# Performance work log

Hardware: AMD Instinct MI355X
Metric: run time of the kernel (lower is better)

The kernel has to match this reference:

```python
import jax, jax.numpy as jnp
import numpy as np

N = 50000   # nodes per graph
E = 800000  # edges per graph
D = 128     # in_dim (num_features)
H = 128     # hidden_channels
R = 8       # num_etypes


def setup_inputs() -> dict:
    key = jax.random.key(0)
    ks = jax.random.split(key, 32)
    inp = {}
    inp["x1"] = jax.random.normal(ks[0], (N, D), dtype=jnp.float32)
    inp["edge_index1"] = jax.random.randint(ks[1], (2, E), 0, N)
    inp["edge_type1"] = jnp.sort(jax.random.randint(ks[2], (E,), 0, R))
    inp["x2"] = jax.random.normal(ks[3], (N, D), dtype=jnp.float32)
    inp["edge_index2"] = jax.random.randint(ks[4], (2, E), 0, N)
    inp["edge_type2"] = jnp.sort(jax.random.randint(ks[5], (E,), 0, R))
    # RGCNConv params: relation weights [R, in, out], root weight [in, out], bias [out]
    dims = [(D, H), (H, H), (H, H)]
    k = 6
    for l, (di, do) in enumerate(dims):
        s = 1.0 / np.sqrt(di)
        inp[f"W{l}"] = jax.random.normal(ks[k], (R, di, do), dtype=jnp.float32) * s; k += 1
        inp[f"root{l}"] = jax.random.normal(ks[k], (di, do), dtype=jnp.float32) * s; k += 1
        inp[f"bias{l}"] = jnp.zeros((do,), dtype=jnp.float32)
    # FCL: MLP on concat(u1, u2) of width 2*H -> H -> 1 (assumed architecture)
    s = 1.0 / np.sqrt(2 * H)
    inp["fc1_w"] = jax.random.normal(ks[k], (2 * H, H), dtype=jnp.float32) * s; k += 1
    inp["fc1_b"] = jnp.zeros((H,), dtype=jnp.float32)
    s = 1.0 / np.sqrt(H)
    inp["fc2_w"] = jax.random.normal(ks[k], (H, 1), dtype=jnp.float32) * s; k += 1
    inp["fc2_b"] = jnp.zeros((1,), dtype=jnp.float32)
    return inp


def rgcn_conv(x, src, dst, etype, W, root, bias):
    # PyG RGCNConv: out_i = root @ x_i + bias + sum_r mean_{j in N_r(i)} W_r x_j
    # transform all nodes by all relation weights: [R, N, H]
    t = jnp.einsum('nd,rdh->rnh', x, W)
    msg = t[etype, src]                       # [E, H] per-edge gathered messages
    comb = dst * R + etype                    # combined (node, relation) segment id
    cnt = jax.ops.segment_sum(jnp.ones((E,), x.dtype), comb, num_segments=N * R)
    msg = msg * (1.0 / jnp.maximum(cnt, 1.0))[comb][:, None]  # per-relation mean norm
    agg = jax.ops.segment_sum(msg, dst, num_segments=N)       # scatter-add over relations
    return agg + x @ root + bias


def gnn(x, edge_index, edge_type, params):
    src, dst = edge_index[0], edge_index[1]
    u = jax.nn.relu(rgcn_conv(x, src, dst, edge_type, *params[0]))
    u = jax.nn.relu(rgcn_conv(u, src, dst, edge_type, *params[1]))
    u = rgcn_conv(u, src, dst, edge_type, *params[2])
    return jnp.mean(u, axis=0).reshape(1, -1)  # [1, H]


def reference(x1, edge_index1, edge_type1, x2, edge_index2, edge_type2,
              W0, root0, bias0, W1, root1, bias1, W2, root2, bias2,
              fc1_w, fc1_b, fc2_w, fc2_b):
    params = [(W0, root0, bias0), (W1, root1, bias1), (W2, root2, bias2)]
    u1 = gnn(x1, edge_index1, edge_type1, params)
    u2 = gnn(x2, edge_index2, edge_type2, params)
    h = jnp.concatenate([u1, u2], axis=-1)    # [1, 2H]
    return jax.nn.relu(h @ fc1_w + fc1_b) @ fc2_w + fc2_b  # [1, 1]
```

## Files before the change

### kernel.cpp

```cpp
#include <hip/hip_runtime.h>

#define R_ET 8
#define DH 128
#define KST 1152
#define GW 1024

typedef __bf16 bf16x8 __attribute__((ext_vector_type(8)));
typedef float f32x4 __attribute__((ext_vector_type(4)));

__device__ __forceinline__ ushort f2bf(float f) {
  unsigned u = __float_as_uint(f);
  u += 0x7fff + ((u >> 16) & 1);
  return (ushort)(u >> 16);
}


__global__ void count_kernel(const int* __restrict__ ei, const int* __restrict__ et,
                             int* __restrict__ cnt, int E) {
  int e = blockIdx.x * blockDim.x + threadIdx.x;
  if (e < E) atomicAdd(&cnt[ei[E + e] * R_ET + et[e]], 1);
}

__global__ __launch_bounds__(1024) void scanA(const int* __restrict__ cnt,
                                              int* __restrict__ off,
                                              int* __restrict__ bsum, int M) {
  __shared__ int s[1024];
  int tid = threadIdx.x;
  int i = blockIdx.x * 1024 + tid;
  int d = (i < M) ? cnt[i] : 0;
  s[tid] = d;
  __syncthreads();
  for (int st = 1; st < 1024; st <<= 1) {
    int v = (tid >= st) ? s[tid - st] : 0;
    __syncthreads();
    s[tid] += v;
    __syncthreads();
  }
  if (i < M) off[i] = s[tid] - d;
  if (tid == 1023) bsum[blockIdx.x] = s[1023];
}

__global__ __launch_bounds__(1024) void scanB(int* __restrict__ bsum, int nb) {
  __shared__ int s[1024];
  int tid = threadIdx.x;
  int v = (tid < nb) ? bsum[tid] : 0;
  s[tid] = v;
  __syncthreads();
  for (int st = 1; st < 1024; st <<= 1) {
    int x = (tid >= st) ? s[tid - st] : 0;
    __syncthreads();
    s[tid] += x;
    __syncthreads();
  }
  if (tid < nb) bsum[tid] = s[tid] - v;
}

__global__ __launch_bounds__(1024) void scanC(int* __restrict__ off,
                                              int* __restrict__ cursor,
                                              const int* __restrict__ bsum,
                                              int M, int E) {
  int i = blockIdx.x * 1024 + threadIdx.x;
  if (i < M) {
    int o = off[i] + bsum[blockIdx.x];
    off[i] = o;
    cursor[i] = o;
  }
  if (i == 0) off[M] = E;
}

__global__ void place_kernel(const int* __restrict__ ei, const int* __restrict__ et,
                             const int* __restrict__ cnt, int* __restrict__ cursor,
                             int2* __restrict__ meta, int E) {
  int e = blockIdx.x * blockDim.x + threadIdx.x;
  if (e >= E) return;
  int src = ei[e], dst = ei[E + e], r = et[e];
  int seg = dst * R_ET + r;
  int slot = atomicAdd(&cursor[seg], 1);
  meta[slot] = make_int2(src, __float_as_int(1.f / (float)cnt[seg]));
}

__global__ __launch_bounds__(256) void wconv_kernel(const float* __restrict__ root,
                                                    const float* __restrict__ W,
                                                    ushort* __restrict__ Wt) {
  int mat = blockIdx.x;
  const float* src = (mat == 8) ? root : (W + (size_t)mat * DH * DH);
  for (int idx = threadIdx.x; idx < DH * DH; idx += 256) {
    int n = idx >> 7, kin = idx & 127;
    int k = mat * DH + kin;
    Wt[(size_t)n * KST + (((k >> 3) ^ (n & 7)) << 3) + (k & 7)] = f2bf(src[kin * DH + n]);
  }
}

__global__ __launch_bounds__(256) void aconv_kernel(const float* __restrict__ src,
                                                    ushort* __restrict__ dst,
                                                    int total, int padtotal) {
  int i4 = (blockIdx.x * 256 + threadIdx.x) * 4;
  if (i4 >= padtotal) return;
  int row = i4 >> 7, k = i4 & 127;
  ushort4 o = make_ushort4(0, 0, 0, 0);
  if (i4 < total) {
    float4 v = *(const float4*)&src[i4];
    o = make_ushort4(f2bf(v.x), f2bf(v.y), f2bf(v.z), f2bf(v.w));
  }
  *(ushort4*)&dst[(size_t)row * DH + (((k >> 3) ^ (row & 7)) << 3) + (k & 7)] = o;
}

__global__ __launch_bounds__(256) void agg_kernel(
    const int* __restrict__ off2, const int2* __restrict__ meta,
    const ushort* __restrict__ Ain, ushort* __restrict__ G, int N, int Npad) {
  int dst = blockIdx.x * 4 + (threadIdx.x >> 6);
  if (dst >= Npad) return;
  int lane = threadIdx.x & 63;
  const int kb = lane >> 2;
  const int klo = (lane * 2) & 7;
  const int swz = dst & 7;

  int offv = 0;
  if (dst < N && lane < 9) offv = off2[dst * R_ET + lane];
  const int s_all = __shfl(offv, 0);
  const int e_end = __shfl(offv, 8);

  float ax[R_ET], ay[R_ET];
#pragma unroll
  for (int r = 0; r < R_ET; r++) { ax[r] = 0.f; ay[r] = 0.f; }

  for (int base = s_all; base < e_end; base += 64) {
    int m = min(64, e_end - base);
    int2 md = make_int2(0, 0);
    if (lane < m) md = meta[base + lane];
#pragma unroll
    for (int r = 0; r < R_ET; r++) {
      int s0 = max(__shfl(offv, r), base);
      int s1 = min(__shfl(offv, r + 1), base + m);
      for (int e = s0; e < s1; e++) {
        int p = __shfl(md.x, e - base);
        float c = __int_as_float(__shfl(md.y, e - base));
        unsigned v = *(const unsigned*)&Ain[((size_t)p << 7) + ((kb ^ (p & 7)) << 3) + klo];
        ax[r] = fmaf(__uint_as_float(v << 16), c, ax[r]);
        ay[r] = fmaf(__uint_as_float(v & 0xffff0000u), c, ay[r]);
      }
    }
  }

  ushort* Grow = G + (size_t)dst * GW;
#pragma unroll
  for (int r = 0; r < R_ET; r++) {
    unsigned o = (unsigned)f2bf(ax[r]) | ((unsigned)f2bf(ay[r]) << 16);
    *(unsigned*)&Grow[(((r * 16 + kb) ^ swz) << 3) + klo] = o;
  }
}

__global__ __launch_bounds__(256) void gemm2(
    const ushort* __restrict__ G, const ushort* __restrict__ Ain,
    const ushort* __restrict__ Wt, const float* __restrict__ bias,
    ushort* __restrict__ Aout, float* __restrict__ pbuf, int N, int last) {
  __shared__ ushort As[128 * DH];
  __shared__ ushort Bs[128 * DH];
  __shared__ float sb[2][DH];
  const int tid = threadIdx.x;
  const int wave = tid >> 6, lane = tid & 63;
  const int quad = lane >> 4, l15 = lane & 15;
  const int rbase = blockIdx.x * 128;
  const int wr = (wave >> 1) * 64, wc = (wave & 1) * 64;

  f32x4 acc[4][4];
#pragma unroll
  for (int i = 0; i < 4; i++)
#pragma unroll
    for (int j = 0; j < 4; j++) acc[i][j] = (f32x4){0.f, 0.f, 0.f, 0.f};

  for (int kc = 0; kc < 9; kc++) {
    if (kc) __syncthreads();
#pragma unroll
    for (int it = 0; it < 4; it++) {
      int i = it * 256 + tid;
      int row = i >> 4, b = i & 15;
      const ushort* srcA = (kc < 8)
          ? G + (size_t)(rbase + row) * GW + kc * 128 + b * 8
          : Ain + (size_t)(rbase + row) * DH + b * 8;
      const ushort* srcB = Wt + (size_t)row * KST + kc * 128 + b * 8;
      __builtin_amdgcn_global_load_lds(
          (const __attribute__((address_space(1))) void*)srcA,
          (__attribute__((address_space(3))) void*)(As + (it * 256 + wave * 64) * 8),
          16, 0, 0);
      __builtin_amdgcn_global_load_lds(
          (const __attribute__((address_space(1))) void*)srcB,
          (__attribute__((address_space(3))) void*)(Bs + (it * 256 + wave * 64) * 8),
          16, 0, 0);
      i += 1024;
      row = i >> 4; b = i & 15;
      srcA = (kc < 8) ? G + (size_t)(rbase + row) * GW + kc * 128 + b * 8
                      : Ain + (size_t)(rbase + row) * DH + b * 8;
      srcB = Wt + (size_t)row * KST + kc * 128 + b * 8;
      __builtin_amdgcn_global_load_lds(
          (const __attribute__((address_space(1))) void*)srcA,
          (__attribute__((address_space(3))) void*)(As + ((it + 4) * 256 + wave * 64) * 8),
          16, 0, 0);
      __builtin_amdgcn_global_load_lds(
          (const __attribute__((address_space(1))) void*)srcB,
          (__attribute__((address_space(3))) void*)(Bs + ((it + 4) * 256 + wave * 64) * 8),
          16, 0, 0);
    }
    __syncthreads();

#pragma unroll
    for (int ks = 0; ks < 4; ks++) {
      bf16x8 af[4], bfr[4];
#pragma unroll
      for (int i = 0; i < 4; i++) {
        int ra = wr + i * 16 + l15;
        int rb = wc + i * 16 + l15;
        af[i] = *(const bf16x8*)&As[ra * DH + (((ks * 4 + quad) ^ (ra & 7)) << 3)];
        bfr[i] = *(const bf16x8*)&Bs[rb * DH + (((ks * 4 + quad) ^ (rb & 7)) << 3)];
      }
#pragma unroll
      for (int i = 0; i < 4; i++)
#pragma unroll
        for (int j = 0; j < 4; j++)
          acc[i][j] = __builtin_amdgcn_mfma_f32_16x16x32_bf16(bfr[j], af[i], acc[i][j], 0, 0, 0);
    }
  }

  if (!last) {
#pragma unroll
    for (int i = 0; i < 4; i++) {
      int node = rbase + wr + i * 16 + l15;
      bool ok = node < N;
#pragma unroll
      for (int j = 0; j < 4; j++) {
        int c0 = wc + j * 16 + quad * 4;
        float4 bv = *(const float4*)&bias[c0];
        unsigned lo = 0, hi = 0;
        if (ok) {
          lo = (unsigned)f2bf(fmaxf(acc[i][j][0] + bv.x, 0.f)) |
               ((unsigned)f2bf(fmaxf(acc[i][j][1] + bv.y, 0.f)) << 16);
          hi = (unsigned)f2bf(fmaxf(acc[i][j][2] + bv.z, 0.f)) |
               ((unsigned)f2bf(fmaxf(acc[i][j][3] + bv.w, 0.f)) << 16);
        }
        *(uint2*)&Aout[(size_t)node * DH + (((c0 >> 3) ^ (node & 7)) << 3) + (c0 & 7)] =
            make_uint2(lo, hi);
      }
    }
  } else {
    if (tid < 2 * DH) ((float*)sb)[tid] = 0.f;
    __syncthreads();
    const int half = wave >> 1;
#pragma unroll
    for (int j = 0; j < 4; j++) {
      f32x4 s;
#pragma unroll
      for (int c = 0; c < 4; c++)
        s[c] = acc[0][j][c] + acc[1][j][c] + acc[2][j][c] + acc[3][j][c];
#pragma unroll
      for (int mask = 1; mask < 16; mask <<= 1)
#pragma unroll
        for (int c = 0; c < 4; c++) s[c] += __shfl_xor(s[c], mask);
      if (l15 == 0) {
        int c0 = wc + j * 16 + quad * 4;
#pragma unroll
        for (int c = 0; c < 4; c++) sb[half][c0 + c] = s[c];
      }
    }
    __syncthreads();
    if (tid < DH) pbuf[(size_t)blockIdx.x * DH + tid] = sb[0][tid] + sb[1][tid];
  }
}

__global__ __launch_bounds__(256) void pool_reduce(const float* __restrict__ pbuf,
                                                   float* __restrict__ u, int nblk) {
  __shared__ float s[256];
  int tid = threadIdx.x;
  int c = tid & 127, h = tid >> 7;
  int chunk = (nblk + gridDim.x - 1) / gridDim.x;
  int r0 = blockIdx.x * chunk;
  int r1 = min(r0 + chunk, nblk);
  float sum = 0.f;
  for (int r = r0 + h; r < r1; r += 2) sum += pbuf[(size_t)r * 128 + c];
  s[tid] = sum;
  __syncthreads();
  if (tid < 128) atomicAdd(&u[c], s[tid] + s[tid + 128]);
}

__global__ __launch_bounds__(256) void mlp_kernel(
    const float* __restrict__ u, const float* __restrict__ b2,
    const float* __restrict__ fc1w, const float* __restrict__ fc1b,
    const float* __restrict__ fc2w, const float* __restrict__ fc2b,
    float* __restrict__ out, int N) {
  __shared__ float uin[256];
  __shared__ float hred[128];
  int tid = threadIdx.x;
  uin[tid] = u[tid] * (1.f / (float)N) + b2[tid & 127];
  __syncthreads();
  if (tid < 128) {
    float s = fc1b[tid];
    for (int i = 0; i < 256; i++) s = fmaf(uin[i], fc1w[i * 128 + tid], s);
    s = fmaxf(s, 0.f);
    hred[tid] = s * fc2w[tid];
  }
  __syncthreads();
  if (tid == 0) {
    float s = fc2b[0];
    for (int i = 0; i < 128; i++) s += hred[i];
    out[0] = s;
  }
}

extern "C" void kernel_launch(void* const* d_in, const int* in_sizes, int n_in,
                              void* d_out, int out_size, void* d_ws, size_t ws_size,
                              hipStream_t stream) {
  const float* x[2] = {(const float*)d_in[0], (const float*)d_in[3]};
  const int* ei[2] = {(const int*)d_in[1], (const int*)d_in[4]};
  const int* et[2] = {(const int*)d_in[2], (const int*)d_in[5]};
  const float* Wp[3] = {(const float*)d_in[6], (const float*)d_in[9], (const float*)d_in[12]};
  const float* rootp[3] = {(const float*)d_in[7], (const float*)d_in[10], (const float*)d_in[13]};
  const float* biasp[3] = {(const float*)d_in[8], (const float*)d_in[11], (const float*)d_in[14]};
  const float* fc1w = (const float*)d_in[15];
  const float* fc1b = (const float*)d_in[16];
  const float* fc2w = (const float*)d_in[17];
  const float* fc2b = (const float*)d_in[18];

  const int N = in_sizes[0] / DH;
  const int E = in_sizes[2];
  const int Npad = (N + 127) & ~127;
  const int ngB = Npad / 128;
  const int M = N * R_ET;
  const int MB = (M + 1023) / 1024;

  char* ws = (char*)d_ws;
  size_t ob = 0;
  auto alloc = [&](size_t bytes) {
    void* p = ws + ob;
    ob = (ob + bytes + 255) & ~(size_t)255;
    return p;
  };
  int* cnt2 = (int*)alloc((size_t)M * 4);
  int* off2 = (int*)alloc((size_t)(M + 1) * 4);
  int* cursor2 = (int*)alloc((size_t)M * 4);
  int* bsum = (int*)alloc(1024 * 4);
  int2* meta = (int2*)alloc((size_t)E * 8);
  float* u = (float*)alloc(1024);
  float* pbuf = (float*)alloc((size_t)ngB * DH * 4);
  ushort* A0 = (ushort*)alloc((size_t)Npad * DH * 2);
  ushort* A1 = (ushort*)alloc((size_t)Npad * DH * 2);
  ushort* G = (ushort*)alloc((size_t)Npad * GW * 2);
  ushort* Wt = (ushort*)alloc((size_t)3 * DH * KST * 2);
  (void)ws_size;

  hipMemsetAsync(u, 0, 2 * DH * sizeof(float), stream);
  for (int l = 0; l < 3; l++)
    wconv_kernel<<<9, 256, 0, stream>>>(rootp[l], Wp[l], Wt + (size_t)l * DH * KST);

  dim3 egrid((E + 255) / 256);
  dim3 nagrid((Npad + 3) / 4);
  const int total = N * DH, padtotal = Npad * DH;
  dim3 agrid((padtotal / 4 + 255) / 256);

  for (int g = 0; g < 2; g++) {
    hipMemsetAsync(cnt2, 0, (size_t)M * sizeof(int), stream);
    count_kernel<<<egrid, 256, 0, stream>>>(ei[g], et[g], cnt2, E);
    scanA<<<MB, 1024, 0, stream>>>(cnt2, off2, bsum, M);
    scanB<<<1, 1024, 0, stream>>>(bsum, MB);
    scanC<<<MB, 1024, 0, stream>>>(off2, cursor2, bsum, M, E);
    place_kernel<<<egrid, 256, 0, stream>>>(ei[g], et[g], cnt2, cursor2, meta, E);
    aconv_kernel<<<agrid, 256, 0, stream>>>(x[g], A0, total, padtotal);

    agg_kernel<<<nagrid, 256, 0, stream>>>(off2, meta, A0, G, N, Npad);
    gemm2<<<ngB, 256, 0, stream>>>(G, A0, Wt, biasp[0], A1, nullptr, N, 0);
    agg_kernel<<<nagrid, 256, 0, stream>>>(off2, meta, A1, G, N, Npad);
    gemm2<<<ngB, 256, 0, stream>>>(G, A1, Wt + (size_t)DH * KST, biasp[1], A0, nullptr, N, 0);
    agg_kernel<<<nagrid, 256, 0, stream>>>(off2, meta, A0, G, N, Npad);
    gemm2<<<ngB, 256, 0, stream>>>(G, A0, Wt + (size_t)2 * DH * KST, nullptr, nullptr, pbuf, N, 1);
    pool_reduce<<<100, 256, 0, stream>>>(pbuf, u + g * DH, ngB);
  }
  mlp_kernel<<<1, 256, 0, stream>>>(u, biasp[2], fc1w, fc1b, fc2w, fc2b,
                                    (float*)d_out, N);
}
```

Baseline: 892.4 us.

## Batch CSR build across both graphs and double-buffer A tiles in GEMM

The count, scan and place steps now run once over both graphs with concatenated segment ids, replacing two separate passes. The three weight-conversion launches are merged into one. In gemm2 the B operand is no longer staged through LDS: fragments are read directly from global Wt. The freed LDS holds a double-buffered A tile, so the next K-chunk loads while the current one computes. This cuts launch count and barrier stalls, at the cost of uncached-by-LDS global reads of B that rely on L1/L2 hits.

```diff
diff --git a/kernel.cpp b/kernel.cpp
--- a/kernel.cpp
+++ b/kernel.cpp
@@ -15,10 +15,16 @@
 }
 
 
-__global__ void count_kernel(const int* __restrict__ ei, const int* __restrict__ et,
-                             int* __restrict__ cnt, int E) {
-  int e = blockIdx.x * blockDim.x + threadIdx.x;
-  if (e < E) atomicAdd(&cnt[ei[E + e] * R_ET + et[e]], 1);
+__global__ void count2_kernel(const int* __restrict__ ei0, const int* __restrict__ et0,
+                              const int* __restrict__ ei1, const int* __restrict__ et1,
+                              int* __restrict__ cnt, int E, int N) {
+  int idx = blockIdx.x * blockDim.x + threadIdx.x;
+  if (idx >= 2 * E) return;
+  int g = idx >= E;
+  int e = idx - (g ? E : 0);
+  const int* ei = g ? ei1 : ei0;
+  const int* et = g ? et1 : et0;
+  atomicAdd(&cnt[(g * N + ei[E + e]) * R_ET + et[e]], 1);
 }
 
 __global__ __launch_bounds__(1024) void scanA(const int* __restrict__ cnt,
@@ -58,36 +64,46 @@
 __global__ __launch_bounds__(1024) void scanC(int* __restrict__ off,
                                               int* __restrict__ cursor,
                                               const int* __restrict__ bsum,
-                                              int M, int E) {
+                                              int M, int E2) {
   int i = blockIdx.x * 1024 + threadIdx.x;
   if (i < M) {
     int o = off[i] + bsum[blockIdx.x];
     off[i] = o;
     cursor[i] = o;
   }
-  if (i == 0) off[M] = E;
-}
-
-__global__ void place_kernel(const int* __restrict__ ei, const int* __restrict__ et,
-                             const int* __restrict__ cnt, int* __restrict__ cursor,
-                             int2* __restrict__ meta, int E) {
-  int e = blockIdx.x * blockDim.x + threadIdx.x;
-  if (e >= E) return;
+  if (i == 0) off[M] = E2;
+}
+
+__global__ void place2_kernel(const int* __restrict__ ei0, const int* __restrict__ et0,
+                              const int* __restrict__ ei1, const int* __restrict__ et1,
+                              const int* __restrict__ cnt, int* __restrict__ cursor,
+                              int2* __restrict__ meta, int E, int N) {
+  int idx = blockIdx.x * blockDim.x + threadIdx.x;
+  if (idx >= 2 * E) return;
+  int g = idx >= E;
+  int e = idx - (g ? E : 0);
+  const int* ei = g ? ei1 : ei0;
+  const int* et = g ? et1 : et0;
   int src = ei[e], dst = ei[E + e], r = et[e];
-  int seg = dst * R_ET + r;
+  int seg = (g * N + dst) * R_ET + r;
   int slot = atomicAdd(&cursor[seg], 1);
   meta[slot] = make_int2(src, __float_as_int(1.f / (float)cnt[seg]));
 }
 
-__global__ __launch_bounds__(256) void wconv_kernel(const float* __restrict__ root,
-                                                    const float* __restrict__ W,
-                                                    ushort* __restrict__ Wt) {
-  int mat = blockIdx.x;
+__global__ __launch_bounds__(256) void wconv_kernel(
+    const float* __restrict__ r0, const float* __restrict__ w0,
+    const float* __restrict__ r1, const float* __restrict__ w1,
+    const float* __restrict__ r2, const float* __restrict__ w2,
+    ushort* __restrict__ Wt) {
+  int l = blockIdx.x / 9, mat = blockIdx.x % 9;
+  const float* root = (l == 0) ? r0 : (l == 1) ? r1 : r2;
+  const float* W = (l == 0) ? w0 : (l == 1) ? w1 : w2;
   const float* src = (mat == 8) ? root : (W + (size_t)mat * DH * DH);
+  ushort* dst = Wt + (size_t)l * DH * KST;
   for (int idx = threadIdx.x; idx < DH * DH; idx += 256) {
     int n = idx >> 7, kin = idx & 127;
     int k = mat * DH + kin;
-    Wt[(size_t)n * KST + (((k >> 3) ^ (n & 7)) << 3) + (k & 7)] = f2bf(src[kin * DH + n]);
+    dst[(size_t)n * KST + (((k >> 3) ^ (n & 7)) << 3) + (k & 7)] = f2bf(src[kin * DH + n]);
   }
 }
 
@@ -154,8 +170,7 @@
     const ushort* __restrict__ G, const ushort* __restrict__ Ain,
     const ushort* __restrict__ Wt, const float* __restrict__ bias,
     ushort* __restrict__ Aout, float* __restrict__ pbuf, int N, int last) {
-  __shared__ ushort As[128 * DH];
-  __shared__ ushort Bs[128 * DH];
+  __shared__ ushort As[2][128 * DH];
   __shared__ float sb[2][DH];
   const int tid = threadIdx.x;
   const int wave = tid >> 6, lane = tid & 63;
@@ -163,55 +178,42 @@
   const int rbase = blockIdx.x * 128;
   const int wr = (wave >> 1) * 64, wc = (wave & 1) * 64;
 
-  f32x4 acc[4][4];
-#pragma unroll
-  for (int i = 0; i < 4; i++)
-#pragma unroll
-    for (int j = 0; j < 4; j++) acc[i][j] = (f32x4){0.f, 0.f, 0.f, 0.f};
-
-  for (int kc = 0; kc < 9; kc++) {
-    if (kc) __syncthreads();
-#pragma unroll
-    for (int it = 0; it < 4; it++) {
+  auto stage = [&](int kc, int buf) {
+#pragma unroll
+    for (int it = 0; it < 8; it++) {
       int i = it * 256 + tid;
       int row = i >> 4, b = i & 15;
       const ushort* srcA = (kc < 8)
           ? G + (size_t)(rbase + row) * GW + kc * 128 + b * 8
           : Ain + (size_t)(rbase + row) * DH + b * 8;
-      const ushort* srcB = Wt + (size_t)row * KST + kc * 128 + b * 8;
       __builtin_amdgcn_global_load_lds(
           (const __attribute__((address_space(1))) void*)srcA,
-          (__attribute__((address_space(3))) void*)(As + (it * 256 + wave * 64) * 8),
+          (__attribute__((address_space(3))) void*)(&As[buf][(it * 256 + wave * 64) * 8]),
           16, 0, 0);
-      __builtin_amdgcn_global_load_lds(
-          (const __attribute__((address_space(1))) void*)srcB,
-          (__attribute__((address_space(3))) void*)(Bs + (it * 256 + wave * 64) * 8),
-          16, 0, 0);
-      i += 1024;
-      row = i >> 4; b = i & 15;
-      srcA = (kc < 8) ? G + (size_t)(rbase + row) * GW + kc * 128 + b * 8
-                      : Ain + (size_t)(rbase + row) * DH + b * 8;
-      srcB = Wt + (size_t)row * KST + kc * 128 + b * 8;
-      __builtin_amdgcn_global_load_lds(
-          (const __attribute__((address_space(1))) void*)srcA,
-          (__attribute__((address_space(3))) void*)(As + ((it + 4) * 256 + wave * 64) * 8),
-          16, 0, 0);
-      __builtin_amdgcn_global_load_lds(
-          (const __attribute__((address_space(1))) void*)srcB,
-          (__attribute__((address_space(3))) void*)(Bs + ((it + 4) * 256 + wave * 64) * 8),
-          16, 0, 0);
-    }
-    __syncthreads();
-
+    }
+  };
+
+  f32x4 acc[4][4];
+#pragma unroll
+  for (int i = 0; i < 4; i++)
+#pragma unroll
+    for (int j = 0; j < 4; j++) acc[i][j] = (f32x4){0.f, 0.f, 0.f, 0.f};
+
+  stage(0, 0);
+  __syncthreads();
+  for (int kc = 0; kc < 9; kc++) {
+    const int buf = kc & 1;
+    if (kc < 8) stage(kc + 1, buf ^ 1);
 #pragma unroll
     for (int ks = 0; ks < 4; ks++) {
+      const int b8 = kc * 16 + ks * 4 + quad;
       bf16x8 af[4], bfr[4];
 #pragma unroll
       for (int i = 0; i < 4; i++) {
         int ra = wr + i * 16 + l15;
         int rb = wc + i * 16 + l15;
-        af[i] = *(const bf16x8*)&As[ra * DH + (((ks * 4 + quad) ^ (ra & 7)) << 3)];
-        bfr[i] = *(const bf16x8*)&Bs[rb * DH + (((ks * 4 + quad) ^ (rb & 7)) << 3)];
+        af[i] = *(const bf16x8*)&As[buf][ra * DH + (((ks * 4 + quad) ^ (ra & 7)) << 3)];
+        bfr[i] = *(const bf16x8*)&Wt[(size_t)rb * KST + ((b8 ^ (rb & 7)) << 3)];
       }
 #pragma unroll
       for (int i = 0; i < 4; i++)
@@ -219,6 +221,7 @@
         for (int j = 0; j < 4; j++)
           acc[i][j] = __builtin_amdgcn_mfma_f32_16x16x32_bf16(bfr[j], af[i], acc[i][j], 0, 0, 0);
     }
+    __syncthreads();
   }
 
   if (!last) {
@@ -323,8 +326,8 @@
   const int E = in_sizes[2];
   const int Npad = (N + 127) & ~127;
   const int ngB = Npad / 128;
-  const int M = N * R_ET;
-  const int MB = (M + 1023) / 1024;
+  const int M2 = 2 * N * R_ET;
+  const int MB2 = (M2 + 1023) / 1024;
 
   char* ws = (char*)d_ws;
   size_t ob = 0;
@@ -333,43 +336,47 @@
     ob = (ob + bytes + 255) & ~(size_t)255;
     return p;
   };
-  int* cnt2 = (int*)alloc((size_t)M * 4);
-  int* off2 = (int*)alloc((size_t)(M + 1) * 4);
-  int* cursor2 = (int*)alloc((size_t)M * 4);
+  int* cnt2 = (int*)alloc((size_t)M2 * 4);
+  int* off2 = (int*)alloc((size_t)(M2 + 1) * 4);
+  int* cursor2 = (int*)alloc((size_t)M2 * 4);
   int* bsum = (int*)alloc(1024 * 4);
-  int2* meta = (int2*)alloc((size_t)E * 8);
+  int2* meta = (int2*)alloc((size_t)2 * E * 8);
   float* u = (float*)alloc(1024);
   float* pbuf = (float*)alloc((size_t)ngB * DH * 4);
   ushort* A0 = (ushort*)alloc((size_t)Npad * DH * 2);
-  ushort* A1 = (ushort*)alloc((size_t)Npad * DH * 2);
+  ushort* B1 = (ushort*)alloc((size_t)Npad * DH * 2);
+  ushort* B2 = (ushort*)alloc((size_t)Npad * DH * 2);
   ushort* G = (ushort*)alloc((size_t)Npad * GW * 2);
   ushort* Wt = (ushort*)alloc((size_t)3 * DH * KST * 2);
   (void)ws_size;
 
   hipMemsetAsync(u, 0, 2 * DH * sizeof(float), stream);
-  for (int l = 0; l < 3; l++)
-    wconv_kernel<<<9, 256, 0, stream>>>(rootp[l], Wp[l], Wt + (size_t)l * DH * KST);
-
-  dim3 egrid((E + 255) / 256);
+  hipMemsetAsync(cnt2, 0, (size_t)M2 * sizeof(int), stream);
+  wconv_kernel<<<27, 256, 0, stream>>>(rootp[0], Wp[0], rootp[1], Wp[1],
+                                       rootp[2], Wp[2], Wt);
+
+  dim3 e2grid((2 * E + 255) / 256);
   dim3 nagrid((Npad + 3) / 4);
   const int total = N * DH, padtotal = Npad * DH;
   dim3 agrid((padtotal / 4 + 255) / 256);
 
+  count2_kernel<<<e2grid, 256, 0, stream>>>(ei[0], et[0], ei[1], et[1], cnt2, E, N);
+  scanA<<<MB2, 1024, 0, stream>>>(cnt2, off2, bsum, M2);
+  scanB<<<1, 1024, 0, stream>>>(bsum, MB2);
+  scanC<<<MB2, 1024, 0, stream>>>(off2, cursor2, bsum, M2, 2 * E);
+  place2_kernel<<<e2grid, 256, 0, stream>>>(ei[0], et[0], ei[1], et[1], cnt2,
+                                            cursor2, meta, E, N);
+
   for (int g = 0; g < 2; g++) {
-    hipMemsetAsync(cnt2, 0, (size_t)M * sizeof(int), stream);
-    count_kernel<<<egrid, 256, 0, stream>>>(ei[g], et[g], cnt2, E);
-    scanA<<<MB, 1024, 0, stream>>>(cnt2, off2, bsum, M);
-    scanB<<<1, 1024, 0, stream>>>(bsum, MB);
-    scanC<<<MB, 1024, 0, stream>>>(off2, cursor2, bsum, M, E);
-    place_kernel<<<egrid, 256, 0, stream>>>(ei[g], et[g], cnt2, cursor2, meta, E);
+    const int* offg = off2 + (size_t)g * N * R_ET;
     aconv_kernel<<<agrid, 256, 0, stream>>>(x[g], A0, total, padtotal);
 
-    agg_kernel<<<nagrid, 256, 0, stream>>>(off2, meta, A0, G, N, Npad);
-    gemm2<<<ngB, 256, 0, stream>>>(G, A0, Wt, biasp[0], A1, nullptr, N, 0);
-    agg_kernel<<<nagrid, 256, 0, stream>>>(off2, meta, A1, G, N, Npad);
-    gemm2<<<ngB, 256, 0, stream>>>(G, A1, Wt + (size_t)DH * KST, biasp[1], A0, nullptr, N, 0);
-    agg_kernel<<<nagrid, 256, 0, stream>>>(off2, meta, A0, G, N, Npad);
-    gemm2<<<ngB, 256, 0, stream>>>(G, A0, Wt + (size_t)2 * DH * KST, nullptr, nullptr, pbuf, N, 1);
+    agg_kernel<<<nagrid, 256, 0, stream>>>(offg, meta, A0, G, N, Npad);
+    gemm2<<<ngB, 256, 0, stream>>>(G, A0, Wt, biasp[0], B1, nullptr, N, 0);
+    agg_kernel<<<nagrid, 256, 0, stream>>>(offg, meta, B1, G, N, Npad);
+    gemm2<<<ngB, 256, 0, stream>>>(G, B1, Wt + (size_t)DH * KST, biasp[1], B2, nullptr, N, 0);
+    agg_kernel<<<nagrid, 256, 0, stream>>>(offg, meta, B2, G, N, Npad);
+    gemm2<<<ngB, 256, 0, stream>>>(G, B2, Wt + (size_t)2 * DH * KST, nullptr, nullptr, pbuf, N, 1);
     pool_reduce<<<100, 256, 0, stream>>>(pbuf, u + g * DH, ngB);
   }
   mlp_kernel<<<1, 256, 0, stream>>>(u, biasp[2], fc1w, fc1b, fc2w, fc2b,
```

New measurement: 909.8 us. No clear change (+2.0%).
